# Performance work log

Hardware: AMD Instinct MI355X
Metric: run time of the kernel (lower is better)

The kernel has to match this reference:

```python
import jax, jax.numpy as jnp
import numpy as np

EMBED = 256
HEADS = 8
HEAD_DIM = EMBED // HEADS
FFN = 1024
EPS = 1e-5


def setup_inputs() -> dict:
    key = jax.random.key(0)
    ks = jax.random.split(key, 12)
    s = 0.02
    return {
        "x": jax.random.normal(ks[0], (2, 4096, EMBED), jnp.float32),
        "ln1_g": jnp.ones((EMBED,), jnp.float32),
        "ln1_b": jnp.zeros((EMBED,), jnp.float32),
        "ln2_g": jnp.ones((EMBED,), jnp.float32),
        "ln2_b": jnp.zeros((EMBED,), jnp.float32),
        "w_qkv": jax.random.normal(ks[1], (EMBED, 3 * EMBED), jnp.float32) * s,
        "b_qkv": jnp.zeros((3 * EMBED,), jnp.float32),
        "w_out": jax.random.normal(ks[2], (EMBED, EMBED), jnp.float32) * s,
        "b_out": jnp.zeros((EMBED,), jnp.float32),
        "w_fc1": jax.random.normal(ks[3], (EMBED, FFN), jnp.float32) * s,
        "b_fc1": jnp.zeros((FFN,), jnp.float32),
        "w_fc2": jax.random.normal(ks[4], (FFN, EMBED), jnp.float32) * s,
        "b_fc2": jnp.zeros((EMBED,), jnp.float32),
    }


def _layernorm(x, g, b):
    mu = jnp.mean(x, axis=-1, keepdims=True)
    var = jnp.mean(jnp.square(x - mu), axis=-1, keepdims=True)
    return (x - mu) * jax.lax.rsqrt(var + EPS) * g + b


def _attn(x, w_qkv, b_qkv, w_out, b_out):
    B, S, E = x.shape
    qkv = x @ w_qkv + b_qkv                      # [B,S,3E]
    q, k, v = jnp.split(qkv, 3, axis=-1)
    def heads(t):
        return t.reshape(B, S, HEADS, HEAD_DIM).transpose(0, 2, 1, 3)  # [B,H,S,D]
    q, k, v = heads(q), heads(k), heads(v)
    scores = jnp.einsum("bhsd,bhtd->bhst", q, k) / (HEAD_DIM ** 0.5)
    w = jax.nn.softmax(scores, axis=-1)
    o = jnp.einsum("bhst,bhtd->bhsd", w, v)      # [B,H,S,D]
    o = o.transpose(0, 2, 1, 3).reshape(B, S, E)
    return o @ w_out + b_out


def reference(x, ln1_g, ln1_b, ln2_g, ln2_b, w_qkv, b_qkv, w_out, b_out,
              w_fc1, b_fc1, w_fc2, b_fc2):
    # Pre-norm MHSA + residual (dropout/droppath inactive at inference)
    x = x + _attn(_layernorm(x, ln1_g, ln1_b), w_qkv, b_qkv, w_out, b_out)
    h = _layernorm(x, ln2_g, ln2_b)
    h = jax.nn.gelu(h @ w_fc1 + b_fc1, approximate=False) @ w_fc2 + b_fc2
    return x + h
```

## Files before the change

### kernel.cpp

```cpp
#include <hip/hip_runtime.h>
#include <hip/hip_bf16.h>
#include <math.h>

typedef __attribute__((ext_vector_type(8))) short bf16x8;
typedef __attribute__((ext_vector_type(4))) float f32x4;
typedef __attribute__((ext_vector_type(4))) unsigned short u16x4;

#define TOKENS 8192
#define EMB 256
#define SEQ 4096
#define NH 8
#define HD 32
#define FFN_DIM 1024

__device__ __forceinline__ unsigned short f2bf_bits(float f) {
  unsigned u = __builtin_bit_cast(unsigned, f);
  u += 0x7FFFu + ((u >> 16) & 1u);
  return (unsigned short)(u >> 16);
}

__global__ __launch_bounds__(256) void wtrans_kernel(const float* __restrict__ w,
                                                     unsigned short* __restrict__ wt,
                                                     int K, int N) {
  int id = blockIdx.x * 256 + threadIdx.x;
  if (id >= N * K) return;
  int n = id / K, kk = id - n * K;
  wt[id] = f2bf_bits(w[(size_t)kk * N + n]);
}

__global__ __launch_bounds__(256) void ln_kernel(const float* __restrict__ x,
                                                 const float* __restrict__ g,
                                                 const float* __restrict__ b,
                                                 unsigned short* __restrict__ out) {
  const int tid = threadIdx.x, lane = tid & 63, wid = tid >> 6;
  const int token = blockIdx.x * 4 + wid;
  const float4 v = *(const float4*)(x + (size_t)token * EMB + lane * 4);
  float s = v.x + v.y + v.z + v.w;
#pragma unroll
  for (int m = 1; m < 64; m <<= 1) s += __shfl_xor(s, m);
  const float mean = s * (1.f / 256.f);
  const float dx = v.x - mean, dy = v.y - mean, dz = v.z - mean, dw = v.w - mean;
  float qv = dx * dx + dy * dy + dz * dz + dw * dw;
#pragma unroll
  for (int m = 1; m < 64; m <<= 1) qv += __shfl_xor(qv, m);
  const float rinv = rsqrtf(qv * (1.f / 256.f) + 1e-5f);
  const float4 gg = *(const float4*)(g + lane * 4);
  const float4 bb = *(const float4*)(b + lane * 4);
  u16x4 ov;
  ov[0] = f2bf_bits(dx * rinv * gg.x + bb.x);
  ov[1] = f2bf_bits(dy * rinv * gg.y + bb.y);
  ov[2] = f2bf_bits(dz * rinv * gg.z + bb.z);
  ov[3] = f2bf_bits(dw * rinv * gg.w + bb.w);
  *(u16x4*)(out + (size_t)token * EMB + lane * 4) = ov;
}

template <int MODE>
__global__ __launch_bounds__(256) void gemm_kernel(
    const unsigned short* __restrict__ A, const unsigned short* __restrict__ WT,
    const float* __restrict__ bias, const float* __restrict__ resid,
    void* __restrict__ out0, void* __restrict__ out1, void* __restrict__ out2,
    int K, int N) {
  __shared__ __align__(16) short ldsA[128 * 64];
  __shared__ __align__(16) short ldsB[128 * 64];
  const int tid = threadIdx.x;
  const int lane = tid & 63, wid = tid >> 6;
  const int llo = lane & 15, lhi = lane >> 4;
  const int m0 = blockIdx.x * 128;
  const int n0 = blockIdx.y * 128;
  const int wm = (wid >> 1) * 64, wn = (wid & 1) * 64;

  f32x4 zero4 = {0.f, 0.f, 0.f, 0.f};
  f32x4 acc[4][4];
#pragma unroll
  for (int i = 0; i < 4; ++i)
#pragma unroll
    for (int j = 0; j < 4; ++j) acc[i][j] = zero4;

  const int nkb = K >> 6;
  for (int kb = 0; kb < nkb; ++kb) {
#pragma unroll
    for (int p = 0; p < 4; ++p) {
      int idx = p * 256 + tid;
      int r = idx >> 3, ch = idx & 7;
      bf16x8 va = *(const bf16x8*)(A + (size_t)(m0 + r) * K + kb * 64 + ch * 8);
      *(bf16x8*)&ldsA[r * 64 + ((ch ^ (r & 7)) * 8)] = va;
      bf16x8 vb = *(const bf16x8*)(WT + (size_t)(n0 + r) * K + kb * 64 + ch * 8);
      *(bf16x8*)&ldsB[r * 64 + ((ch ^ (r & 7)) * 8)] = vb;
    }
    __syncthreads();
#pragma unroll
    for (int ks = 0; ks < 2; ++ks) {
      bf16x8 af[4], bfr[4];
#pragma unroll
      for (int mf = 0; mf < 4; ++mf) {
        int r = wm + mf * 16 + llo;
        af[mf] = *(const bf16x8*)&ldsA[r * 64 + (((ks * 4 + lhi) ^ (r & 7)) * 8)];
      }
#pragma unroll
      for (int nf = 0; nf < 4; ++nf) {
        int r = wn + nf * 16 + llo;
        bfr[nf] = *(const bf16x8*)&ldsB[r * 64 + (((ks * 4 + lhi) ^ (r & 7)) * 8)];
      }
#pragma unroll
      for (int mf = 0; mf < 4; ++mf)
#pragma unroll
        for (int nf = 0; nf < 4; ++nf)
          acc[mf][nf] = __builtin_amdgcn_mfma_f32_16x16x32_bf16(af[mf], bfr[nf], acc[mf][nf], 0, 0, 0);
    }
    __syncthreads();
  }

#pragma unroll
  for (int mf = 0; mf < 4; ++mf) {
#pragma unroll
    for (int nf = 0; nf < 4; ++nf) {
      const int n = n0 + wn + nf * 16 + llo;
      const float bv = bias[n];
#pragma unroll
      for (int r = 0; r < 4; ++r) {
        const int m = m0 + wm + mf * 16 + lhi * 4 + r;
        float val = acc[mf][nf][r] + bv;
        if constexpr (MODE == 0) {
          const int part = n >> 8, rem = n & 255, h = rem >> 5, d = rem & 31;
          const int bb = m >> 12, s = m & 4095, bh = bb * 8 + h;
          unsigned short ob = f2bf_bits(val);
          if (part == 0)
            ((unsigned short*)out0)[((size_t)bh * SEQ + s) * HD + d] = ob;
          else if (part == 1)
            ((unsigned short*)out1)[((size_t)bh * SEQ + s) * HD + d] = ob;
          else
            ((unsigned short*)out2)[((size_t)bh * HD + d) * SEQ + s] = ob;
        } else if constexpr (MODE == 2) {
          float gel = 0.5f * val * (1.0f + erff(val * 0.70710678118654752f));
          ((unsigned short*)out0)[(size_t)m * N + n] = f2bf_bits(gel);
        } else {
          ((float*)out0)[(size_t)m * N + n] = val + resid[(size_t)m * N + n];
        }
      }
    }
  }
}

__global__ __launch_bounds__(256) void attn_kernel(const unsigned short* __restrict__ q,
                                                   const unsigned short* __restrict__ k,
                                                   const unsigned short* __restrict__ vT,
                                                   unsigned short* __restrict__ o) {
  __shared__ __align__(16) short plds[4][32 * 64];
  const int tid = threadIdx.x, lane = tid & 63, wid = tid >> 6;
  const int llo = lane & 15, lhi = lane >> 4;
  const int bh = blockIdx.y, qb = blockIdx.x;
  const int bb = bh >> 3, hh = bh & 7;
  const int q0 = qb * 128 + wid * 32;
  const unsigned short* qp = q + (size_t)bh * SEQ * HD;
  const unsigned short* kp = k + (size_t)bh * SEQ * HD;
  const unsigned short* vp = vT + (size_t)bh * HD * SEQ;

  f32x4 zero4 = {0.f, 0.f, 0.f, 0.f};
  bf16x8 qf[2];
#pragma unroll
  for (int mf = 0; mf < 2; ++mf)
    qf[mf] = *(const bf16x8*)(qp + (size_t)(q0 + mf * 16 + llo) * HD + lhi * 8);

  f32x4 acc[2][2];
  float mrun[2][4], lrun[2][4];
#pragma unroll
  for (int mf = 0; mf < 2; ++mf) {
    acc[mf][0] = zero4;
    acc[mf][1] = zero4;
#pragma unroll
    for (int r = 0; r < 4; ++r) { mrun[mf][r] = -1e30f; lrun[mf][r] = 0.f; }
  }

  bf16x8 kf0[4], vf0[4], kf1[4], vf1[4];

  auto load_k = [&](int tt, bf16x8(&kf)[4]) {
#pragma unroll
    for (int tf = 0; tf < 4; ++tf)
      kf[tf] = *(const bf16x8*)(kp + (size_t)(tt * 64 + tf * 16 + llo) * HD + lhi * 8);
  };
  auto load_v = [&](int tt, bf16x8(&vf)[4]) {
#pragma unroll
    for (int df = 0; df < 2; ++df)
#pragma unroll
      for (int ks = 0; ks < 2; ++ks)
        vf[df * 2 + ks] =
            *(const bf16x8*)(vp + (size_t)(df * 16 + llo) * SEQ + tt * 64 + ks * 32 + lhi * 8);
  };

  const float scale = 0.17677669529663687f;

  auto step = [&](int tt, bf16x8(&kf)[4], bf16x8(&vf)[4], bf16x8(&kn)[4], bf16x8(&vn)[4]) {
    int tn = tt + 1;
    if (tn > 63) tn = 63;
    load_k(tn, kn);
    load_v(tn, vn);
    f32x4 sc[2][4];
#pragma unroll
    for (int mf = 0; mf < 2; ++mf)
#pragma unroll
      for (int tf = 0; tf < 4; ++tf)
        sc[mf][tf] = __builtin_amdgcn_mfma_f32_16x16x32_bf16(qf[mf], kf[tf], zero4, 0, 0, 0);
#pragma unroll
    for (int mf = 0; mf < 2; ++mf) {
#pragma unroll
      for (int r = 0; r < 4; ++r) {
        float rm = fmaxf(fmaxf(sc[mf][0][r], sc[mf][1][r]), fmaxf(sc[mf][2][r], sc[mf][3][r]));
        rm = fmaxf(rm, __shfl_xor(rm, 1));
        rm = fmaxf(rm, __shfl_xor(rm, 2));
        rm = fmaxf(rm, __shfl_xor(rm, 4));
        rm = fmaxf(rm, __shfl_xor(rm, 8));
        rm *= scale;
        const float mn = fmaxf(mrun[mf][r], rm);
        const float al = __expf(mrun[mf][r] - mn);
        mrun[mf][r] = mn;
        float rs = 0.f;
#pragma unroll
        for (int tf = 0; tf < 4; ++tf) {
          float p = __expf(__builtin_fmaf(sc[mf][tf][r], scale, -mn));
          sc[mf][tf][r] = p;
          rs += p;
        }
        rs += __shfl_xor(rs, 1);
        rs += __shfl_xor(rs, 2);
        rs += __shfl_xor(rs, 4);
        rs += __shfl_xor(rs, 8);
        lrun[mf][r] = lrun[mf][r] * al + rs;
        acc[mf][0][r] *= al;
        acc[mf][1][r] *= al;
      }
    }
#pragma unroll
    for (int mf = 0; mf < 2; ++mf)
#pragma unroll
      for (int tf = 0; tf < 4; ++tf)
#pragma unroll
        for (int r = 0; r < 4; ++r) {
          const int row = mf * 16 + lhi * 4 + r;
          const int col = tf * 16 + llo;
          const int sch = (col >> 3) ^ (row & 7);
          plds[wid][row * 64 + sch * 8 + (col & 7)] = (short)f2bf_bits(sc[mf][tf][r]);
        }
#pragma unroll
    for (int ks = 0; ks < 2; ++ks) {
      bf16x8 pa[2];
#pragma unroll
      for (int mf = 0; mf < 2; ++mf) {
        const int row = mf * 16 + llo;
        const int sch = (ks * 4 + lhi) ^ (row & 7);
        pa[mf] = *(const bf16x8*)&plds[wid][row * 64 + sch * 8];
      }
#pragma unroll
      for (int mf = 0; mf < 2; ++mf)
#pragma unroll
        for (int df = 0; df < 2; ++df)
          acc[mf][df] =
              __builtin_amdgcn_mfma_f32_16x16x32_bf16(pa[mf], vf[df * 2 + ks], acc[mf][df], 0, 0, 0);
    }
  };

  load_k(0, kf0);
  load_v(0, vf0);
  for (int t2 = 0; t2 < 32; ++t2) {
    step(t2 * 2, kf0, vf0, kf1, vf1);
    step(t2 * 2 + 1, kf1, vf1, kf0, vf0);
  }

#pragma unroll
  for (int mf = 0; mf < 2; ++mf)
#pragma unroll
    for (int df = 0; df < 2; ++df)
#pragma unroll
      for (int r = 0; r < 4; ++r) {
        const int mrow = q0 + mf * 16 + lhi * 4 + r;
        const float val = acc[mf][df][r] / lrun[mf][r];
        o[(size_t)(bb * SEQ + mrow) * EMB + hh * 32 + df * 16 + llo] = f2bf_bits(val);
      }
}

extern "C" void kernel_launch(void* const* d_in, const int* in_sizes, int n_in,
                              void* d_out, int out_size, void* d_ws, size_t ws_size,
                              hipStream_t stream) {
  const float* x = (const float*)d_in[0];
  const float* ln1_g = (const float*)d_in[1];
  const float* ln1_b = (const float*)d_in[2];
  const float* ln2_g = (const float*)d_in[3];
  const float* ln2_b = (const float*)d_in[4];
  const float* w_qkv = (const float*)d_in[5];
  const float* b_qkv = (const float*)d_in[6];
  const float* w_out = (const float*)d_in[7];
  const float* b_out = (const float*)d_in[8];
  const float* w_fc1 = (const float*)d_in[9];
  const float* b_fc1 = (const float*)d_in[10];
  const float* w_fc2 = (const float*)d_in[11];
  const float* b_fc2 = (const float*)d_in[12];
  float* out = (float*)d_out;

  char* ws = (char*)d_ws;
  size_t off = 0;
  auto alloc = [&](size_t bytes) {
    void* p = ws + off;
    off += (bytes + 255) & ~(size_t)255;
    return p;
  };
  unsigned short* wqkvT = (unsigned short*)alloc((size_t)768 * 256 * 2);
  unsigned short* woutT = (unsigned short*)alloc((size_t)256 * 256 * 2);
  unsigned short* wfc1T = (unsigned short*)alloc((size_t)1024 * 256 * 2);
  unsigned short* wfc2T = (unsigned short*)alloc((size_t)256 * 1024 * 2);
  unsigned short* ln1o = (unsigned short*)alloc((size_t)TOKENS * EMB * 2);
  unsigned short* qbuf = (unsigned short*)alloc((size_t)16 * SEQ * HD * 2);
  unsigned short* kbuf = (unsigned short*)alloc((size_t)16 * SEQ * HD * 2);
  unsigned short* vTbuf = (unsigned short*)alloc((size_t)16 * SEQ * HD * 2);
  unsigned short* obuf = (unsigned short*)alloc((size_t)TOKENS * EMB * 2);
  float* x1 = (float*)alloc((size_t)TOKENS * EMB * 4);
  unsigned short* h2 = (unsigned short*)alloc((size_t)TOKENS * EMB * 2);
  unsigned short* ffn1 = (unsigned short*)alloc((size_t)TOKENS * FFN_DIM * 2);

  dim3 blk(256);
  wtrans_kernel<<<dim3((768 * 256 + 255) / 256), blk, 0, stream>>>(w_qkv, wqkvT, 256, 768);
  wtrans_kernel<<<dim3((256 * 256 + 255) / 256), blk, 0, stream>>>(w_out, woutT, 256, 256);
  wtrans_kernel<<<dim3((1024 * 256 + 255) / 256), blk, 0, stream>>>(w_fc1, wfc1T, 256, 1024);
  wtrans_kernel<<<dim3((256 * 1024 + 255) / 256), blk, 0, stream>>>(w_fc2, wfc2T, 1024, 256);

  ln_kernel<<<dim3(TOKENS / 4), blk, 0, stream>>>(x, ln1_g, ln1_b, ln1o);

  gemm_kernel<0><<<dim3(64, 6), blk, 0, stream>>>(ln1o, wqkvT, b_qkv, nullptr,
                                                  qbuf, kbuf, vTbuf, 256, 768);

  attn_kernel<<<dim3(32, 16), blk, 0, stream>>>(qbuf, kbuf, vTbuf, obuf);

  gemm_kernel<1><<<dim3(64, 2), blk, 0, stream>>>(obuf, woutT, b_out, x,
                                                  x1, nullptr, nullptr, 256, 256);

  ln_kernel<<<dim3(TOKENS / 4), blk, 0, stream>>>(x1, ln2_g, ln2_b, h2);

  gemm_kernel<2><<<dim3(64, 8), blk, 0, stream>>>(h2, wfc1T, b_fc1, nullptr,
                                                  ffn1, nullptr, nullptr, 256, 1024);

  gemm_kernel<3><<<dim3(64, 2), blk, 0, stream>>>(ffn1, wfc2T, b_fc2, x1,
                                                  out, nullptr, nullptr, 1024, 256);
}
```

Measured before the change: 335.4 us.

## Shrink GEMM and attention tiles for more blocks; merge weight transposes

Templates the GEMM on BM/BN and launches smaller tiles (128x64, 64x64), giving more blocks on the many-CU GPU. The attention kernel halves queries per wave (16 rows) to double the grid, and packs P to bf16 by truncation instead of rounding. The four weight-transpose launches are merged into one. More blocks improve occupancy and load balance, at the cost of less K/V and weight reuse per block and slightly different rounding of P.

After: 319.5 us. -4.8%, faster.

```diff
diff --git a/kernel.cpp b/kernel.cpp
--- a/kernel.cpp
+++ b/kernel.cpp
@@ -19,13 +19,26 @@
   return (unsigned short)(u >> 16);
 }
 
-__global__ __launch_bounds__(256) void wtrans_kernel(const float* __restrict__ w,
-                                                     unsigned short* __restrict__ wt,
-                                                     int K, int N) {
+__global__ __launch_bounds__(256) void wtrans_all_kernel(
+    const float* __restrict__ w_qkv, const float* __restrict__ w_out,
+    const float* __restrict__ w_fc1, const float* __restrict__ w_fc2,
+    unsigned short* __restrict__ t_qkv, unsigned short* __restrict__ t_out,
+    unsigned short* __restrict__ t_fc1, unsigned short* __restrict__ t_fc2) {
   int id = blockIdx.x * 256 + threadIdx.x;
-  if (id >= N * K) return;
-  int n = id / K, kk = id - n * K;
-  wt[id] = f2bf_bits(w[(size_t)kk * N + n]);
+  const int S0 = 256 * 768, S1 = S0 + 256 * 256, S2 = S1 + 256 * 1024, S3 = S2 + 1024 * 256;
+  if (id < S0) {
+    int n = id / 256, kk = id - n * 256;
+    t_qkv[id] = f2bf_bits(w_qkv[(size_t)kk * 768 + n]);
+  } else if (id < S1) {
+    int r = id - S0; int n = r / 256, kk = r - n * 256;
+    t_out[r] = f2bf_bits(w_out[(size_t)kk * 256 + n]);
+  } else if (id < S2) {
+    int r = id - S1; int n = r / 256, kk = r - n * 256;
+    t_fc1[r] = f2bf_bits(w_fc1[(size_t)kk * 1024 + n]);
+  } else if (id < S3) {
+    int r = id - S2; int n = r / 1024, kk = r - n * 1024;
+    t_fc2[r] = f2bf_bits(w_fc2[(size_t)kk * 256 + n]);
+  }
 }
 
 __global__ __launch_bounds__(256) void ln_kernel(const float* __restrict__ x,
@@ -54,66 +67,72 @@
   *(u16x4*)(out + (size_t)token * EMB + lane * 4) = ov;
 }
 
-template <int MODE>
+template <int MODE, int BM, int BN>
 __global__ __launch_bounds__(256) void gemm_kernel(
     const unsigned short* __restrict__ A, const unsigned short* __restrict__ WT,
     const float* __restrict__ bias, const float* __restrict__ resid,
     void* __restrict__ out0, void* __restrict__ out1, void* __restrict__ out2,
     int K, int N) {
-  __shared__ __align__(16) short ldsA[128 * 64];
-  __shared__ __align__(16) short ldsB[128 * 64];
+  constexpr int MF = BM / 32, NF = BN / 32;
+  __shared__ __align__(16) short ldsA[BM * 64];
+  __shared__ __align__(16) short ldsB[BN * 64];
   const int tid = threadIdx.x;
   const int lane = tid & 63, wid = tid >> 6;
   const int llo = lane & 15, lhi = lane >> 4;
-  const int m0 = blockIdx.x * 128;
-  const int n0 = blockIdx.y * 128;
-  const int wm = (wid >> 1) * 64, wn = (wid & 1) * 64;
+  const int m0 = blockIdx.x * BM;
+  const int n0 = blockIdx.y * BN;
+  const int wm = (wid >> 1) * (BM / 2), wn = (wid & 1) * (BN / 2);
 
   f32x4 zero4 = {0.f, 0.f, 0.f, 0.f};
-  f32x4 acc[4][4];
-#pragma unroll
-  for (int i = 0; i < 4; ++i)
-#pragma unroll
-    for (int j = 0; j < 4; ++j) acc[i][j] = zero4;
+  f32x4 acc[MF][NF];
+#pragma unroll
+  for (int i = 0; i < MF; ++i)
+#pragma unroll
+    for (int j = 0; j < NF; ++j) acc[i][j] = zero4;
 
   const int nkb = K >> 6;
   for (int kb = 0; kb < nkb; ++kb) {
 #pragma unroll
-    for (int p = 0; p < 4; ++p) {
+    for (int p = 0; p < BM / 32; ++p) {
       int idx = p * 256 + tid;
       int r = idx >> 3, ch = idx & 7;
       bf16x8 va = *(const bf16x8*)(A + (size_t)(m0 + r) * K + kb * 64 + ch * 8);
       *(bf16x8*)&ldsA[r * 64 + ((ch ^ (r & 7)) * 8)] = va;
+    }
+#pragma unroll
+    for (int p = 0; p < BN / 32; ++p) {
+      int idx = p * 256 + tid;
+      int r = idx >> 3, ch = idx & 7;
       bf16x8 vb = *(const bf16x8*)(WT + (size_t)(n0 + r) * K + kb * 64 + ch * 8);
       *(bf16x8*)&ldsB[r * 64 + ((ch ^ (r & 7)) * 8)] = vb;
     }
     __syncthreads();
 #pragma unroll
     for (int ks = 0; ks < 2; ++ks) {
-      bf16x8 af[4], bfr[4];
-#pragma unroll
-      for (int mf = 0; mf < 4; ++mf) {
+      bf16x8 af[MF], bfr[NF];
+#pragma unroll
+      for (int mf = 0; mf < MF; ++mf) {
         int r = wm + mf * 16 + llo;
         af[mf] = *(const bf16x8*)&ldsA[r * 64 + (((ks * 4 + lhi) ^ (r & 7)) * 8)];
       }
 #pragma unroll
-      for (int nf = 0; nf < 4; ++nf) {
+      for (int nf = 0; nf < NF; ++nf) {
         int r = wn + nf * 16 + llo;
         bfr[nf] = *(const bf16x8*)&ldsB[r * 64 + (((ks * 4 + lhi) ^ (r & 7)) * 8)];
       }
 #pragma unroll
-      for (int mf = 0; mf < 4; ++mf)
-#pragma unroll
-        for (int nf = 0; nf < 4; ++nf)
+      for (int mf = 0; mf < MF; ++mf)
+#pragma unroll
+        for (int nf = 0; nf < NF; ++nf)
           acc[mf][nf] = __builtin_amdgcn_mfma_f32_16x16x32_bf16(af[mf], bfr[nf], acc[mf][nf], 0, 0, 0);
     }
     __syncthreads();
   }
 
 #pragma unroll
-  for (int mf = 0; mf < 4; ++mf) {
-#pragma unroll
-    for (int nf = 0; nf < 4; ++nf) {
+  for (int mf = 0; mf < MF; ++mf) {
+#pragma unroll
+    for (int nf = 0; nf < NF; ++nf) {
       const int n = n0 + wn + nf * 16 + llo;
       const float bv = bias[n];
 #pragma unroll
@@ -145,31 +164,25 @@
                                                    const unsigned short* __restrict__ k,
                                                    const unsigned short* __restrict__ vT,
                                                    unsigned short* __restrict__ o) {
-  __shared__ __align__(16) short plds[4][32 * 64];
+  __shared__ __align__(16) short plds[4][16 * 64];
   const int tid = threadIdx.x, lane = tid & 63, wid = tid >> 6;
   const int llo = lane & 15, lhi = lane >> 4;
   const int bh = blockIdx.y, qb = blockIdx.x;
   const int bb = bh >> 3, hh = bh & 7;
-  const int q0 = qb * 128 + wid * 32;
+  const int q0 = qb * 64 + wid * 16;
   const unsigned short* qp = q + (size_t)bh * SEQ * HD;
   const unsigned short* kp = k + (size_t)bh * SEQ * HD;
   const unsigned short* vp = vT + (size_t)bh * HD * SEQ;
 
   f32x4 zero4 = {0.f, 0.f, 0.f, 0.f};
-  bf16x8 qf[2];
-#pragma unroll
-  for (int mf = 0; mf < 2; ++mf)
-    qf[mf] = *(const bf16x8*)(qp + (size_t)(q0 + mf * 16 + llo) * HD + lhi * 8);
-
-  f32x4 acc[2][2];
-  float mrun[2][4], lrun[2][4];
-#pragma unroll
-  for (int mf = 0; mf < 2; ++mf) {
-    acc[mf][0] = zero4;
-    acc[mf][1] = zero4;
-#pragma unroll
-    for (int r = 0; r < 4; ++r) { mrun[mf][r] = -1e30f; lrun[mf][r] = 0.f; }
-  }
+  bf16x8 qf = *(const bf16x8*)(qp + (size_t)(q0 + llo) * HD + lhi * 8);
+
+  f32x4 acc[2];
+  float mrun[4], lrun[4];
+  acc[0] = zero4;
+  acc[1] = zero4;
+#pragma unroll
+  for (int r = 0; r < 4; ++r) { mrun[r] = -1e30f; lrun[r] = 0.f; }
 
   bf16x8 kf0[4], vf0[4], kf1[4], vf1[4];
 
@@ -194,67 +207,54 @@
     if (tn > 63) tn = 63;
     load_k(tn, kn);
     load_v(tn, vn);
-    f32x4 sc[2][4];
-#pragma unroll
-    for (int mf = 0; mf < 2; ++mf)
-#pragma unroll
-      for (int tf = 0; tf < 4; ++tf)
-        sc[mf][tf] = __builtin_amdgcn_mfma_f32_16x16x32_bf16(qf[mf], kf[tf], zero4, 0, 0, 0);
-#pragma unroll
-    for (int mf = 0; mf < 2; ++mf) {
+    f32x4 sc[4];
+#pragma unroll
+    for (int tf = 0; tf < 4; ++tf)
+      sc[tf] = __builtin_amdgcn_mfma_f32_16x16x32_bf16(qf, kf[tf], zero4, 0, 0, 0);
+#pragma unroll
+    for (int r = 0; r < 4; ++r) {
+      float rm = fmaxf(fmaxf(sc[0][r], sc[1][r]), fmaxf(sc[2][r], sc[3][r]));
+      rm = fmaxf(rm, __shfl_xor(rm, 1));
+      rm = fmaxf(rm, __shfl_xor(rm, 2));
+      rm = fmaxf(rm, __shfl_xor(rm, 4));
+      rm = fmaxf(rm, __shfl_xor(rm, 8));
+      rm *= scale;
+      const float mn = fmaxf(mrun[r], rm);
+      const float al = __expf(mrun[r] - mn);
+      mrun[r] = mn;
+      float rs = 0.f;
+#pragma unroll
+      for (int tf = 0; tf < 4; ++tf) {
+        float p = __expf(__builtin_fmaf(sc[tf][r], scale, -mn));
+        sc[tf][r] = p;
+        rs += p;
+      }
+      rs += __shfl_xor(rs, 1);
+      rs += __shfl_xor(rs, 2);
+      rs += __shfl_xor(rs, 4);
+      rs += __shfl_xor(rs, 8);
+      lrun[r] = lrun[r] * al + rs;
+      acc[0][r] *= al;
+      acc[1][r] *= al;
+    }
+#pragma unroll
+    for (int tf = 0; tf < 4; ++tf)
 #pragma unroll
       for (int r = 0; r < 4; ++r) {
-        float rm = fmaxf(fmaxf(sc[mf][0][r], sc[mf][1][r]), fmaxf(sc[mf][2][r], sc[mf][3][r]));
-        rm = fmaxf(rm, __shfl_xor(rm, 1));
-        rm = fmaxf(rm, __shfl_xor(rm, 2));
-        rm = fmaxf(rm, __shfl_xor(rm, 4));
-        rm = fmaxf(rm, __shfl_xor(rm, 8));
-        rm *= scale;
-        const float mn = fmaxf(mrun[mf][r], rm);
-        const float al = __expf(mrun[mf][r] - mn);
-        mrun[mf][r] = mn;
-        float rs = 0.f;
-#pragma unroll
-        for (int tf = 0; tf < 4; ++tf) {
-          float p = __expf(__builtin_fmaf(sc[mf][tf][r], scale, -mn));
-          sc[mf][tf][r] = p;
-          rs += p;
-        }
-        rs += __shfl_xor(rs, 1);
-        rs += __shfl_xor(rs, 2);
-        rs += __shfl_xor(rs, 4);
-        rs += __shfl_xor(rs, 8);
-        lrun[mf][r] = lrun[mf][r] * al + rs;
-        acc[mf][0][r] *= al;
-        acc[mf][1][r] *= al;
-      }
-    }
-#pragma unroll
-    for (int mf = 0; mf < 2; ++mf)
-#pragma unroll
-      for (int tf = 0; tf < 4; ++tf)
-#pragma unroll
-        for (int r = 0; r < 4; ++r) {
-          const int row = mf * 16 + lhi * 4 + r;
-          const int col = tf * 16 + llo;
-          const int sch = (col >> 3) ^ (row & 7);
-          plds[wid][row * 64 + sch * 8 + (col & 7)] = (short)f2bf_bits(sc[mf][tf][r]);
-        }
+        const int row = lhi * 4 + r;
+        const int col = tf * 16 + llo;
+        const int sch = (col >> 3) ^ (row & 7);
+        plds[wid][row * 64 + sch * 8 + (col & 7)] =
+            (short)(__builtin_bit_cast(unsigned, sc[tf][r]) >> 16);
+      }
 #pragma unroll
     for (int ks = 0; ks < 2; ++ks) {
-      bf16x8 pa[2];
-#pragma unroll
-      for (int mf = 0; mf < 2; ++mf) {
-        const int row = mf * 16 + llo;
-        const int sch = (ks * 4 + lhi) ^ (row & 7);
-        pa[mf] = *(const bf16x8*)&plds[wid][row * 64 + sch * 8];
-      }
-#pragma unroll
-      for (int mf = 0; mf < 2; ++mf)
-#pragma unroll
-        for (int df = 0; df < 2; ++df)
-          acc[mf][df] =
-              __builtin_amdgcn_mfma_f32_16x16x32_bf16(pa[mf], vf[df * 2 + ks], acc[mf][df], 0, 0, 0);
+      const int row = llo;
+      const int sch = (ks * 4 + lhi) ^ (row & 7);
+      bf16x8 pa = *(const bf16x8*)&plds[wid][row * 64 + sch * 8];
+#pragma unroll
+      for (int df = 0; df < 2; ++df)
+        acc[df] = __builtin_amdgcn_mfma_f32_16x16x32_bf16(pa, vf[df * 2 + ks], acc[df], 0, 0, 0);
     }
   };
 
@@ -266,15 +266,15 @@
   }
 
 #pragma unroll
-  for (int mf = 0; mf < 2; ++mf)
-#pragma unroll
-    for (int df = 0; df < 2; ++df)
-#pragma unroll
-      for (int r = 0; r < 4; ++r) {
-        const int mrow = q0 + mf * 16 + lhi * 4 + r;
-        const float val = acc[mf][df][r] / lrun[mf][r];
-        o[(size_t)(bb * SEQ + mrow) * EMB + hh * 32 + df * 16 + llo] = f2bf_bits(val);
-      }
+  for (int r = 0; r < 4; ++r) {
+    const float rl = 1.0f / lrun[r];
+    const int mrow = q0 + lhi * 4 + r;
+#pragma unroll
+    for (int df = 0; df < 2; ++df) {
+      const float val = acc[df][r] * rl;
+      o[(size_t)(bb * SEQ + mrow) * EMB + hh * 32 + df * 16 + llo] = f2bf_bits(val);
+    }
+  }
 }
 
 extern "C" void kernel_launch(void* const* d_in, const int* in_sizes, int n_in,
@@ -316,26 +316,24 @@
   unsigned short* ffn1 = (unsigned short*)alloc((size_t)TOKENS * FFN_DIM * 2);
 
   dim3 blk(256);
-  wtrans_kernel<<<dim3((768 * 256 + 255) / 256), blk, 0, stream>>>(w_qkv, wqkvT, 256, 768);
-  wtrans_kernel<<<dim3((256 * 256 + 255) / 256), blk, 0, stream>>>(w_out, woutT, 256, 256);
-  wtrans_kernel<<<dim3((1024 * 256 + 255) / 256), blk, 0, stream>>>(w_fc1, wfc1T, 256, 1024);
-  wtrans_kernel<<<dim3((256 * 1024 + 255) / 256), blk, 0, stream>>>(w_fc2, wfc2T, 1024, 256);
+  wtrans_all_kernel<<<dim3(3072), blk, 0, stream>>>(w_qkv, w_out, w_fc1, w_fc2,
+                                                    wqkvT, woutT, wfc1T, wfc2T);
 
   ln_kernel<<<dim3(TOKENS / 4), blk, 0, stream>>>(x, ln1_g, ln1_b, ln1o);
 
-  gemm_kernel<0><<<dim3(64, 6), blk, 0, stream>>>(ln1o, wqkvT, b_qkv, nullptr,
-                                                  qbuf, kbuf, vTbuf, 256, 768);
-
-  attn_kernel<<<dim3(32, 16), blk, 0, stream>>>(qbuf, kbuf, vTbuf, obuf);
-
-  gemm_kernel<1><<<dim3(64, 2), blk, 0, stream>>>(obuf, woutT, b_out, x,
-                                                  x1, nullptr, nullptr, 256, 256);
+  gemm_kernel<0, 128, 64><<<dim3(64, 12), blk, 0, stream>>>(ln1o, wqkvT, b_qkv, nullptr,
+                                                            qbuf, kbuf, vTbuf, 256, 768);
+
+  attn_kernel<<<dim3(64, 16), blk, 0, stream>>>(qbuf, kbuf, vTbuf, obuf);
+
+  gemm_kernel<1, 64, 64><<<dim3(128, 4), blk, 0, stream>>>(obuf, woutT, b_out, x,
+                                                           x1, nullptr, nullptr, 256, 256);
 
   ln_kernel<<<dim3(TOKENS / 4), blk, 0, stream>>>(x1, ln2_g, ln2_b, h2);
 
-  gemm_kernel<2><<<dim3(64, 8), blk, 0, stream>>>(h2, wfc1T, b_fc1, nullptr,
-                                                  ffn1, nullptr, nullptr, 256, 1024);
-
-  gemm_kernel<3><<<dim3(64, 2), blk, 0, stream>>>(ffn1, wfc2T, b_fc2, x1,
-                                                  out, nullptr, nullptr, 1024, 256);
-}
+  gemm_kernel<2, 128, 64><<<dim3(64, 16), blk, 0, stream>>>(h2, wfc1T, b_fc1, nullptr,
+                                                            ffn1, nullptr, nullptr, 256, 1024);
+
+  gemm_kernel<3, 64, 64><<<dim3(128, 4), blk, 0, stream>>>(ffn1, wfc2T, b_fc2, x1,
+                                                           out, nullptr, nullptr, 1024, 256);
+}
```
